# Optimization experiments

Measured on AMD Instinct MI355X. Metric: run time of the kernel, lower is better.

## Reference

```python
import jax, jax.numpy as jnp
import numpy as np

C_CURV = 0.01
K = 20
BALL_EPS = 4e-3  # hyptorch float32 boundary eps


def _e2p(x, c=C_CURV):
    # ToPoincare: expmap0 then project onto the Poincare ball
    sqrt_c = c ** 0.5
    n = jnp.maximum(jnp.linalg.norm(x, axis=-1, keepdims=True), 1e-15)
    y = jnp.tanh(sqrt_c * n) * x / (sqrt_c * n)
    maxnorm = (1.0 - BALL_EPS) / sqrt_c
    ny = jnp.maximum(jnp.linalg.norm(y, axis=-1, keepdims=True), 1e-15)
    return jnp.where(ny > maxnorm, y * (maxnorm / ny), y)


def _mobius_add(x, y, c=C_CURV):
    x2 = jnp.sum(x * x, axis=-1, keepdims=True)
    y2 = jnp.sum(y * y, axis=-1, keepdims=True)
    xy = jnp.sum(x * y, axis=-1, keepdims=True)
    num = (1.0 + 2.0 * c * xy + c * y2) * x + (1.0 - c * x2) * y
    den = 1.0 + 2.0 * c * xy + c * c * x2 * y2
    return num / jnp.maximum(den, 1e-15)


def _knn(x, k):
    # x: (B, C, N); Euclidean negative squared distance, topk indices
    inner = -2.0 * jnp.einsum('bcn,bcm->bnm', x, x)
    xx = jnp.sum(x * x, axis=1)  # (B, N)
    pd = -xx[:, :, None] - inner - xx[:, None, :]
    return jax.lax.top_k(pd, k)[1]  # (B, N, k)


def _graph_feature(x, k=K):
    # x: (B, C, N) -> (B, 2C, N, k)
    idx = _knn(x, k)
    xp = _e2p(jnp.transpose(x, (0, 2, 1)))  # (B, N, C) on Poincare ball
    feat = jax.vmap(lambda xb, ib: xb[ib])(xp, idx)  # (B, N, k, C) gather
    xc = jnp.broadcast_to(xp[:, :, None, :], feat.shape)
    out = jnp.concatenate([_mobius_add(feat, -xc), xc], axis=-1)
    return jnp.transpose(out, (0, 3, 1, 2))


def _bn(x, g, b, axes, eps=1e-5):
    # BatchNorm (training-mode batch statistics), channel axis = 1
    m = jnp.mean(x, axis=axes, keepdims=True)
    v = jnp.mean((x - m) ** 2, axis=axes, keepdims=True)
    shp = [1] * x.ndim
    shp[1] = -1
    return (x - m) / jnp.sqrt(v + eps) * g.reshape(shp) + b.reshape(shp)


def _ln(x, g, b, eps=1e-5):
    m = jnp.mean(x, axis=-1, keepdims=True)
    v = jnp.mean((x - m) ** 2, axis=-1, keepdims=True)
    return (x - m) / jnp.sqrt(v + eps) * g + b


def setup_inputs() -> dict:
    key = jax.random.key(0)
    ks = jax.random.split(key, 8)
    B, N, OUT = 16, 1024, 40
    s = 0.05
    return {
        'x': jax.random.normal(ks[0], (B, N, 3), jnp.float32),
        'conv1_w': jax.random.normal(ks[1], (64, 6), jnp.float32) * s,
        'bn1_g': jnp.ones((64,), jnp.float32), 'bn1_b': jnp.zeros((64,), jnp.float32),
        'conv2_w': jax.random.normal(ks[2], (192, 128), jnp.float32) * s,
        'bn2_g': jnp.ones((192,), jnp.float32), 'bn2_b': jnp.zeros((192,), jnp.float32),
        'conv3_w': jax.random.normal(ks[3], (1024, 256), jnp.float32) * s,
        'bn3_g': jnp.ones((1024,), jnp.float32), 'bn3_b': jnp.zeros((1024,), jnp.float32),
        'fc1_w': jax.random.normal(ks[4], (512, 1024), jnp.float32) * s,
        'fc1_b': jnp.zeros((512,), jnp.float32),
        'ln1_g': jnp.ones((512,), jnp.float32), 'ln1_b': jnp.zeros((512,), jnp.float32),
        'fc2_w': jax.random.normal(ks[5], (256, 512), jnp.float32) * s,
        'fc2_b': jnp.zeros((256,), jnp.float32),
        'ln2_g': jnp.ones((256,), jnp.float32), 'ln2_b': jnp.zeros((256,), jnp.float32),
        'out_w': jax.random.normal(ks[6], (OUT, 256), jnp.float32) * s,
        'out_b': jnp.zeros((OUT,), jnp.float32),
    }


def reference(x, conv1_w, bn1_g, bn1_b, conv2_w, bn2_g, bn2_b,
              conv3_w, bn3_g, bn3_b, fc1_w, fc1_b, ln1_g, ln1_b,
              fc2_w, fc2_b, ln2_g, ln2_b, out_w, out_b):
    xt = jnp.transpose(x, (0, 2, 1))  # (B, 3, N)
    f = _graph_feature(xt)            # (B, 6, N, k)
    h = jnp.einsum('oc,bcnk->bonk', conv1_w, f)
    h = jax.nn.relu(_bn(h, bn1_g, bn1_b, (0, 2, 3)))
    x1 = jnp.max(h, axis=-1)          # (B, 64, N)
    f = _graph_feature(x1)            # (B, 128, N, k)
    h = jnp.einsum('oc,bcnk->bonk', conv2_w, f)
    h = jax.nn.relu(_bn(h, bn2_g, bn2_b, (0, 2, 3)))
    x2 = jnp.max(h, axis=-1)          # (B, 192, N)
    h = jnp.concatenate([x1, x2], axis=1)  # (B, 256, N)
    h = jnp.einsum('oc,bcn->bon', conv3_w, h)
    h = jax.nn.relu(_bn(h, bn3_g, bn3_b, (0, 2)))
    h = jnp.max(h, axis=-1)           # (B, 1024)
    h = jax.nn.relu(_ln(h @ fc1_w.T + fc1_b, ln1_g, ln1_b))
    h = jax.nn.relu(_ln(h @ fc2_w.T + fc2_b, ln2_g, ln2_b))
    logits = h @ out_w.T + out_b      # (B, outdim)
    return jax.nn.log_softmax(logits, axis=1)
```

## Files before the change

kernel.cpp:

```cpp
#include <hip/hip_runtime.h>
#include <math.h>

#define B_ 16
#define N_ 1024
#define KNN 20
#define NPAIR (B_*N_)

typedef __attribute__((ext_vector_type(8))) short bf16x8;
typedef __attribute__((ext_vector_type(4))) float f32x4;

__device__ __forceinline__ unsigned fkey(float f) {
  unsigned u = __float_as_uint(f);
  return (u & 0x80000000u) ? ~u : (u | 0x80000000u);
}
__device__ __forceinline__ float fkeyinv(unsigned u) {
  unsigned b = (u & 0x80000000u) ? (u ^ 0x80000000u) : ~u;
  return __uint_as_float(b);
}
__device__ __forceinline__ unsigned short f2bf(float x) {
  unsigned u = __float_as_uint(x);
  unsigned r = (u + 0x7FFFu + ((u >> 16) & 1u)) >> 16;
  return (unsigned short)r;
}
__device__ __forceinline__ float bf2f(unsigned short u) {
  return __uint_as_float(((unsigned)u) << 16);
}
__device__ __forceinline__ unsigned knnkey(float d, int idx) {
  return (fkey(d) & 0xFFFFFC00u) | (unsigned)(1023 - idx);
}

__device__ __forceinline__ void topk_insert_u32(unsigned (&kl)[KNN], unsigned nk) {
  kl[KNN-1] = nk;
  #pragma unroll
  for (int i = KNN-1; i > 0; i--) {
    unsigned hi = max(kl[i-1], kl[i]);
    unsigned lo = min(kl[i-1], kl[i]);
    kl[i-1] = hi; kl[i] = lo;
  }
}

__device__ __forceinline__ int cnt_gt(const unsigned* __restrict__ L, unsigned v) {
  int j = 0;
  #pragma unroll
  for (int s = 16; s; s >>= 1) {
    int nj = j + s;
    if (nj <= KNN && L[nj-1] > v) j = nj;
  }
  return j;
}

__global__ void __launch_bounds__(256) k_prep_knn1(const float* __restrict__ x,
        float* __restrict__ xp1, const float* __restrict__ w2, const float* __restrict__ w3,
        unsigned short* __restrict__ w2h, unsigned short* __restrict__ wt3h,
        unsigned* __restrict__ keypart) {
  __shared__ float P[N_*3];
  __shared__ float XX[N_];
  if (blockIdx.x >= 512) {
    int i = (blockIdx.x - 512) * 256 + threadIdx.x;
    if (i < NPAIR) {
      float a0 = x[i*3+0], a1 = x[i*3+1], a2 = x[i*3+2];
      float n = sqrtf(a0*a0 + a1*a1 + a2*a2);
      n = fmaxf(n, 1e-15f);
      float th = tanhf(0.1f * n);
      float sc = th / (0.1f * n);
      float ny = fmaxf(th * 10.0f, 1e-15f);
      float mxn = (1.0f - 4e-3f) / 0.1f;
      if (ny > mxn) sc *= mxn / ny;
      xp1[i*3+0] = sc*a0; xp1[i*3+1] = sc*a1; xp1[i*3+2] = sc*a2;
    }
    if (i < 192*128) w2h[i] = f2bf(w2[i]);
    wt3h[i] = f2bf(w3[i]);
    return;
  }
  int blk = blockIdx.x;
  int b = blk >> 5, rc = (blk >> 3) & 3, cc = blk & 7;
  const float* xb = x + b*N_*3;
  for (int e = threadIdx.x; e < N_*3; e += 256) P[e] = xb[e];
  __syncthreads();
  for (int j = threadIdx.x; j < N_; j += 256) {
    float q0 = P[j*3], q1 = P[j*3+1], q2 = P[j*3+2];
    XX[j] = q0*q0 + q1*q1 + q2*q2;
  }
  __syncthreads();
  int r = rc*256 + threadIdx.x;
  float q0 = P[r*3], q1 = P[r*3+1], q2 = P[r*3+2];
  float xxq = XX[r];
  unsigned kl[KNN];
  #pragma unroll
  for (int i = 0; i < KNN; i++) kl[i] = 0u;
  int cbase = cc*128;
  for (int jj = 0; jj < 128; jj++) {
    int j = cbase + jj;
    float dot = q0*P[j*3] + q1*P[j*3+1] + q2*P[j*3+2];
    float d = 2.0f*dot - xxq - XX[j];
    unsigned nk = knnkey(d, j);
    if (nk > kl[KNN-1]) topk_insert_u32(kl, nk);
  }
  int p = b*N_ + r;
  unsigned* pe = keypart + (size_t)p*160 + cc*20;
  #pragma unroll
  for (int i = 0; i < KNN; i++) pe[i] = kl[i];
}

__global__ void __launch_bounds__(256) k_conv1(const float* __restrict__ xp1,
                        const unsigned* __restrict__ keypart,
                        const float* __restrict__ w1, float* __restrict__ hmax1,
                        float* __restrict__ hmin1, double* __restrict__ stats1sh) {
  __shared__ float F[4][KNN][6];
  __shared__ float red[4][64][2];
  __shared__ int idxs[16][KNN];
  __shared__ unsigned keybuf[2560];
  __shared__ unsigned out1[1280];
  __shared__ unsigned out2[640];
  int g = threadIdx.x >> 6, lane = threadIdx.x & 63;
  int tid = threadIdx.x;
  int pbase = blockIdx.x * 16;
  {
    const unsigned* src = keypart + (size_t)pbase*160;
    for (int e = tid; e < 2560; e += 256) keybuf[e] = src[e];
  }
  float w[6];
  #pragma unroll
  for (int c = 0; c < 6; c++) w[c] = w1[lane*6 + c];
  __syncthreads();
  for (int e = tid; e < 2560; e += 256) {
    int pt = e / 160, rem = e - pt*160;
    int m = rem / 40, i = rem - m*40;
    const unsigned* A = keybuf + pt*160 + (2*m)*20;
    const unsigned* Bl = A + 20;
    unsigned v; const unsigned* S; int own;
    if (i < 20) { v = A[i]; S = Bl; own = i; }
    else { v = Bl[i-20]; S = A; own = i-20; }
    int rank = own + cnt_gt(S, v);
    if (rank < KNN) out1[(pt*4 + m)*20 + rank] = v;
  }
  __syncthreads();
  for (int e = tid; e < 1280; e += 256) {
    int pt = e / 80, rem = e - pt*80;
    int m2 = rem / 40, i = rem - m2*40;
    const unsigned* A = out1 + (pt*4 + 2*m2)*20;
    const unsigned* Bl = A + 20;
    unsigned v; const unsigned* S; int own;
    if (i < 20) { v = A[i]; S = Bl; own = i; }
    else { v = Bl[i-20]; S = A; own = i-20; }
    int rank = own + cnt_gt(S, v);
    if (rank < KNN) out2[(pt*2 + m2)*20 + rank] = v;
  }
  __syncthreads();
  for (int e = tid; e < 640; e += 256) {
    int pt = e / 40, i = e - pt*40;
    const unsigned* A = out2 + pt*40;
    const unsigned* Bl = A + 20;
    unsigned v; const unsigned* S; int own;
    if (i < 20) { v = A[i]; S = Bl; own = i; }
    else { v = Bl[i-20]; S = A; own = i-20; }
    int rank = own + cnt_gt(S, v);
    if (rank < KNN) idxs[pt][rank] = 1023 - (int)(v & 1023u);
  }
  float sum = 0.f, sumsq = 0.f;
  __syncthreads();
  for (int it = 0; it < 4; ++it) {
    int p = pbase + it*4 + g;
    if (lane < KNN) {
      int nb = idxs[it*4 + g][lane];
      int bb = p >> 10;
      const float* xc = xp1 + p*3;
      const float* ft = xp1 + (bb*N_ + nb)*3;
      float x0 = ft[0], x1 = ft[1], x2v = ft[2];
      float c0 = xc[0], c1 = xc[1], c2 = xc[2];
      float X2 = x0*x0 + x1*x1 + x2v*x2v;
      float Y2 = c0*c0 + c1*c1 + c2*c2;
      float XY = -(x0*c0 + x1*c1 + x2v*c2);
      float den = fmaxf(1.0f + 0.02f*XY + 1e-4f*X2*Y2, 1e-15f);
      float s1 = (1.0f + 0.02f*XY + 0.01f*Y2) / den;
      float s2 = (1.0f - 0.01f*X2) / den;
      F[g][lane][0] = s1*x0 - s2*c0;
      F[g][lane][1] = s1*x1 - s2*c1;
      F[g][lane][2] = s1*x2v - s2*c2;
      F[g][lane][3] = c0; F[g][lane][4] = c1; F[g][lane][5] = c2;
    }
    __syncthreads();
    float mx = -__builtin_inff(), mn = __builtin_inff();
    for (int k = 0; k < KNN; k++) {
      float h = 0.f;
      #pragma unroll
      for (int c = 0; c < 6; c++) h = fmaf(w[c], F[g][k][c], h);
      mx = fmaxf(mx, h); mn = fminf(mn, h);
      sum += h; sumsq += h*h;
    }
    hmax1[(pbase + it*4 + g)*64 + lane] = mx;
    hmin1[(pbase + it*4 + g)*64 + lane] = mn;
    __syncthreads();
  }
  red[g][lane][0] = sum; red[g][lane][1] = sumsq;
  __syncthreads();
  if (g == 0) {
    float s  = red[0][lane][0] + red[1][lane][0] + red[2][lane][0] + red[3][lane][0];
    float s2 = red[0][lane][1] + red[1][lane][1] + red[2][lane][1] + red[3][lane][1];
    double* dst = stats1sh + ((size_t)(blockIdx.x & 63)*64 + lane)*2;
    atomicAdd(dst, (double)s);
    atomicAdd(dst + 1, (double)s2);
  }
}

__global__ void __launch_bounds__(64) k_bn_reduce(const double* __restrict__ sh, int nch, int nslots,
                            double cnt,
                            const float* __restrict__ g, const float* __restrict__ bb,
                            float* __restrict__ scale, float* __restrict__ shift) {
  int o = blockIdx.x, t = threadIdx.x;
  double s = 0.0, s2 = 0.0;
  for (int sl = t; sl < nslots; sl += 64) {
    s  += sh[((size_t)sl*nch + o)*2];
    s2 += sh[((size_t)sl*nch + o)*2 + 1];
  }
  #pragma unroll
  for (int off = 32; off > 0; off >>= 1) { s += __shfl_xor(s, off); s2 += __shfl_xor(s2, off); }
  if (t == 0) {
    double m = s / cnt;
    double v = s2 / cnt - m*m;
    float a = g[o] / sqrtf((float)v + 1e-5f);
    scale[o] = a;
    shift[o] = bb[o] - a * (float)m;
  }
}

__global__ void __launch_bounds__(256) k_bn1_apply(const float* __restrict__ hmax1, const float* __restrict__ hmin1,
                            const float* __restrict__ scale1, const float* __restrict__ shift1,
                            float* __restrict__ xp2,
                            unsigned short* __restrict__ x1h, unsigned short* __restrict__ x1l,
                            float* __restrict__ xx1) {
  int b = blockIdx.x >> 4, nc = blockIdx.x & 15;
  int c = threadIdx.x & 63, sub = threadIdx.x >> 6;
  int n0 = nc*64 + sub*16;
  float a = scale1[c], t = shift1[c];
  #pragma unroll
  for (int i = 0; i < 16; i++) {
    int p = b*1024 + n0 + i;
    float h = (a >= 0.f) ? hmax1[(size_t)p*64 + c] : hmin1[(size_t)p*64 + c];
    float x1 = fmaxf(fmaf(a, h, t), 0.f);
    unsigned short hb = f2bf(x1);
    x1h[(size_t)p*64 + c] = hb;
    x1l[(size_t)p*64 + c] = f2bf(x1 - bf2f(hb));
    float n2 = x1*x1;
    #pragma unroll
    for (int off = 32; off > 0; off >>= 1) n2 += __shfl_xor(n2, off);
    if (c == 0) xx1[p] = n2;
    float n1 = fmaxf(sqrtf(n2), 1e-15f);
    float th = tanhf(0.1f * n1);
    float sc = th / (0.1f * n1);
    float ny = fmaxf(th * 10.0f, 1e-15f);
    float mxn = (1.0f - 4e-3f) / 0.1f;
    if (ny > mxn) sc *= mxn / ny;
    xp2[(size_t)p*64 + c] = sc * x1;
  }
}

__global__ void __launch_bounds__(256) k_knn2g(const unsigned short* __restrict__ x1h,
        const unsigned short* __restrict__ x1l,
        const float* __restrict__ xx1, unsigned* __restrict__ keypart2) {
  __shared__ __align__(16) float SM[4096];
  int tid = threadIdx.x;
  int bi = blockIdx.x;
  int blk = ((bi & 7) << 7) + (bi >> 3);
  int b = blk >> 6, qc = (blk >> 2) & 15, cc = blk & 3;
  int qbase = qc*64, ccbase = cc*256;
  int wave = tid >> 6, lane = tid & 63;
  int lm = lane & 15, kq = lane >> 4;
  const size_t base = (size_t)b * 65536;

  bf16x8 Qh[4][2], Ql[4][2];
  #pragma unroll
  for (int qt = 0; qt < 4; qt++) {
    size_t ro = base + (size_t)(qbase + qt*16 + lm)*64 + kq*8;
    #pragma unroll
    for (int ks = 0; ks < 2; ks++) {
      Qh[qt][ks] = *((const bf16x8*)(x1h + ro + ks*32));
      Ql[qt][ks] = *((const bf16x8*)(x1l + ro + ks*32));
    }
  }
  unsigned kl[KNN];
  #pragma unroll
  for (int i = 0; i < KNN; i++) kl[i] = 0u;
  int cq = lane + (lane >> 2);

  for (int st = 0; st < 4; ++st) {
    int cb0 = ccbase + st*64;
    size_t co = base + (size_t)(cb0 + wave*16 + lm)*64 + kq*8;
    bf16x8 Ah[2], Al[2];
    #pragma unroll
    for (int ks = 0; ks < 2; ks++) {
      Ah[ks] = *((const bf16x8*)(x1h + co + ks*32));
      Al[ks] = *((const bf16x8*)(x1l + co + ks*32));
    }
    float4 xxc = *((const float4*)(xx1 + b*1024 + cb0 + wave*16 + kq*4));
    f32x4 acc[4];
    #pragma unroll
    for (int qt = 0; qt < 4; qt++) acc[qt] = (f32x4){0.f, 0.f, 0.f, 0.f};
    #pragma unroll
    for (int ks = 0; ks < 2; ks++) {
      #pragma unroll
      for (int qt = 0; qt < 4; qt++) {
        acc[qt] = __builtin_amdgcn_mfma_f32_16x16x32_bf16(Ah[ks], Qh[qt][ks], acc[qt], 0, 0, 0);
        acc[qt] = __builtin_amdgcn_mfma_f32_16x16x32_bf16(Ah[ks], Ql[qt][ks], acc[qt], 0, 0, 0);
        acc[qt] = __builtin_amdgcn_mfma_f32_16x16x32_bf16(Al[ks], Qh[qt][ks], acc[qt], 0, 0, 0);
        acc[qt] = __builtin_amdgcn_mfma_f32_16x16x32_bf16(Al[ks], Ql[qt][ks], acc[qt], 0, 0, 0);
      }
    }
    __syncthreads();
    float xxcv[4] = {xxc.x, xxc.y, xxc.z, xxc.w};
    #pragma unroll
    for (int qt = 0; qt < 4; qt++) {
      int q = qt*16 + lm;
      #pragma unroll
      for (int r = 0; r < 4; r++) {
        int c = wave*16 + kq*4 + r;
        SM[q*64 + ((c + q + (q>>2)) & 63)] = 2.0f*acc[qt][r] - xxcv[r];
      }
    }
    __syncthreads();
    #pragma unroll
    for (int j = 0; j < 16; j++) {
      int c = wave*16 + j;
      float d = SM[lane*64 + ((c + cq) & 63)];
      unsigned nk = knnkey(d, cb0 + c);
      if (nk > kl[KNN-1]) topk_insert_u32(kl, nk);
    }
  }
  __syncthreads();
  unsigned* U = (unsigned*)SM;
  unsigned* L0 = U;
  unsigned* L1 = U + 1344;
  unsigned* M  = U + 2688;
  if (wave == 0) {
    #pragma unroll
    for (int i = 0; i < KNN; i++) L0[lane*21 + i] = kl[i];
  } else if (wave == 1) {
    #pragma unroll
    for (int i = 0; i < KNN; i++) L1[lane*21 + i] = kl[i];
  }
  __syncthreads();
  if (tid < 64) {
    int ia = 0, ib = 0;
    for (int t = 0; t < KNN; t++) {
      unsigned pa = L0[tid*21 + ia], pb = L1[tid*21 + ib];
      bool ta = pa > pb;
      M[tid*21 + t] = ta ? pa : pb;
      if (ta) ia++; else ib++;
    }
  }
  __syncthreads();
  if (wave == 2) {
    #pragma unroll
    for (int i = 0; i < KNN; i++) L0[lane*21 + i] = kl[i];
  } else if (wave == 3) {
    #pragma unroll
    for (int i = 0; i < KNN; i++) L1[lane*21 + i] = kl[i];
  }
  __syncthreads();
  if (tid < 64) {
    int p = b*N_ + qbase + tid;
    unsigned* pe = keypart2 + (size_t)p*80 + cc*20;
    int ia = 0, ib = 0, im = 0;
    for (int t = 0; t < KNN; t++) {
      unsigned pa = L0[tid*21 + ia], pb = L1[tid*21 + ib], pm = M[tid*21 + im];
      unsigned bp = pm; int sel = 2;
      if (pa > bp) { bp = pa; sel = 0; }
      if (pb > bp) { bp = pb; sel = 1; }
      pe[t] = bp;
      if (sel == 0) ia++; else if (sel == 1) ib++; else im++;
    }
  }
}

__global__ void __launch_bounds__(256) k_conv2m(const float* __restrict__ xp2,
    const unsigned* __restrict__ keypart2, const unsigned short* __restrict__ w2h,
    float* __restrict__ hmax2, float* __restrict__ hmin2, double* __restrict__ stats2sh) {
  __shared__ __align__(16) short Abf[80*136];
  __shared__ __align__(16) float Cf[4][64];
  __shared__ float Yc[4];
  __shared__ int nbr[80];
  __shared__ unsigned keybuf[320];
  int tid = threadIdx.x;
  int bi = blockIdx.x;
  int g512 = ((bi & 7) << 9) + (bi >> 3);
  int p0 = g512 * 4;
  int b = p0 >> 10;
  for (int e = tid; e < 320; e += 256) keybuf[e] = keypart2[(size_t)p0*80 + e];
  if (tid < 64) {
    int pt = tid >> 4, qq = tid & 15;
    float4 cv = *((const float4*)(xp2 + (size_t)(p0 + pt)*64) + qq);
    *((float4*)&Cf[pt][qq*4]) = cv;
    float y2 = cv.x*cv.x + cv.y*cv.y + cv.z*cv.z + cv.w*cv.w;
    #pragma unroll
    for (int off = 8; off > 0; off >>= 1) y2 += __shfl_xor(y2, off);
    if (qq == 0) Yc[pt] = y2;
    ushort4 cb;
    cb.x = f2bf(cv.x); cb.y = f2bf(cv.y); cb.z = f2bf(cv.z); cb.w = f2bf(cv.w);
    #pragma unroll
    for (int a = 0; a < 5; a++)
      #pragma unroll
      for (int j2 = 0; j2 < 4; j2++)
        *((ushort4*)(Abf + (a*16 + pt*4 + j2)*136 + 64 + qq*4)) = cb;
  }
  __syncthreads();
  for (int e = tid; e < 320; e += 256) {
    int pt = e / 80;
    int rem = e - pt*80;
    int c = rem / 20;
    int i = rem - c*20;
    const unsigned* LB = keybuf + pt*80;
    unsigned v = LB[c*20 + i];
    int rank = i;
    #pragma unroll
    for (int c2 = 0; c2 < 4; c2++) {
      if (c2 == c) continue;
      rank += cnt_gt(LB + c2*20, v);
    }
    if (rank < KNN) nbr[pt*20 + rank] = 1023 - (int)(v & 1023u);
  }
  __syncthreads();
  for (int e = tid; e < 80*16; e += 256) {
    int r = e >> 4, qq = e & 15;
    int q = (r >> 2) & 3;
    int L = 20*q + 4*(r >> 4) + (r & 3);
    float4 f = *((const float4*)(xp2 + (size_t)(b*N_ + nbr[L])*64) + qq);
    float4 cvf = *((const float4*)&Cf[q][qq*4]);
    float X2 = f.x*f.x + f.y*f.y + f.z*f.z + f.w*f.w;
    float XY = -(f.x*cvf.x + f.y*cvf.y + f.z*cvf.z + f.w*cvf.w);
    #pragma unroll
    for (int off = 8; off > 0; off >>= 1) {
      X2 += __shfl_xor(X2, off);
      XY += __shfl_xor(XY, off);
    }
    float Y2 = Yc[q];
    float den = fmaxf(1.0f + 0.02f*XY + 1e-4f*X2*Y2, 1e-15f);
    float inv = 1.0f / den;
    float s1 = (1.0f + 0.02f*XY + 0.01f*Y2) * inv;
    float s2 = (1.0f - 0.01f*X2) * inv;
    ushort4 mo;
    mo.x = f2bf(s1*f.x - s2*cvf.x);
    mo.y = f2bf(s1*f.y - s2*cvf.y);
    mo.z = f2bf(s1*f.z - s2*cvf.z);
    mo.w = f2bf(s1*f.w - s2*cvf.w);
    *((ushort4*)(Abf + r*136 + qq*4)) = mo;
  }
  __syncthreads();
  int wave = tid >> 6, lane = tid & 63;
  int quad = lane >> 4, lm = lane & 15;
  int colbase = wave*48;
  f32x4 acc[5][3];
  #pragma unroll
  for (int rt = 0; rt < 5; rt++)
    #pragma unroll
    for (int cj = 0; cj < 3; cj++) acc[rt][cj] = (f32x4){0.f, 0.f, 0.f, 0.f};
  #pragma unroll
  for (int kt = 0; kt < 4; kt++) {
    int k0 = kt*32 + quad*8;
    bf16x8 bf[3];
    #pragma unroll
    for (int cj = 0; cj < 3; cj++)
      bf[cj] = *((const bf16x8*)(w2h + (size_t)(colbase + cj*16 + lm)*128 + k0));
    bf16x8 af[5];
    #pragma unroll
    for (int rt = 0; rt < 5; rt++)
      af[rt] = *((const bf16x8*)(Abf + (rt*16 + lm)*136 + k0));
    #pragma unroll
    for (int rt = 0; rt < 5; rt++)
      #pragma unroll
      for (int cj = 0; cj < 3; cj++)
        acc[rt][cj] = __builtin_amdgcn_mfma_f32_16x16x32_bf16(af[rt], bf[cj], acc[rt][cj], 0, 0, 0);
  }
  #pragma unroll
  for (int cj = 0; cj < 3; cj++) {
    int o = colbase + cj*16 + lm;
    float s = 0.f, s2 = 0.f, mx = -__builtin_inff(), mn = __builtin_inff();
    #pragma unroll
    for (int rt = 0; rt < 5; rt++) {
      #pragma unroll
      for (int reg = 0; reg < 4; reg++) {
        float h = acc[rt][cj][reg];
        s += h; s2 += h*h;
        mx = fmaxf(mx, h); mn = fminf(mn, h);
      }
    }
    hmax2[(size_t)(p0 + quad)*192 + o] = mx;
    hmin2[(size_t)(p0 + quad)*192 + o] = mn;
    s  += __shfl_xor(s, 16);  s  += __shfl_xor(s, 32);
    s2 += __shfl_xor(s2, 16); s2 += __shfl_xor(s2, 32);
    if (lane < 16) {
      double* dst = stats2sh + ((size_t)(bi & 255)*192 + o)*2;
      atomicAdd(dst, (double)s); atomicAdd(dst + 1, (double)s2);
    }
  }
}

__global__ void __launch_bounds__(256) k_conv3m(
   const float* __restrict__ hmax1, const float* __restrict__ hmin1,
   const float* __restrict__ scale1, const float* __restrict__ shift1,
   const float* __restrict__ hmax2, const float* __restrict__ hmin2,
   const float* __restrict__ scale2, const float* __restrict__ shift2,
   const unsigned short* __restrict__ wt3h, double* __restrict__ stats3sh,
   unsigned* __restrict__ hmax3u, unsigned* __restrict__ hmin3u) {
  __shared__ short As[64*264];
  int tid = threadIdx.x;
  int mt = blockIdx.x >> 2, cb = blockIdx.x & 3;
  int rowbase = mt*64;
  int b = rowbase >> 10;
  int c4 = tid & 63;
  float4 sc, sh;
  if (c4 < 16) {
    sc = *((const float4*)(scale1 + c4*4));
    sh = *((const float4*)(shift1 + c4*4));
  } else {
    sc = *((const float4*)(scale2 + (c4*4 - 64)));
    sh = *((const float4*)(shift2 + (c4*4 - 64)));
  }
  #pragma unroll 4
  for (int i = 0; i < 16; i++) {
    int r = (tid >> 6) + i*4;
    int p = rowbase + r;
    float4 hx, hn;
    if (c4 < 16) {
      hx = *((const float4*)(hmax1 + (size_t)p*64 + c4*4));
      hn = *((const float4*)(hmin1 + (size_t)p*64 + c4*4));
    } else {
      hx = *((const float4*)(hmax2 + (size_t)p*192 + (c4*4 - 64)));
      hn = *((const float4*)(hmin2 + (size_t)p*192 + (c4*4 - 64)));
    }
    ushort4 o4;
    o4.x = f2bf(fmaxf(fmaf(sc.x, (sc.x >= 0.f ? hx.x : hn.x), sh.x), 0.f));
    o4.y = f2bf(fmaxf(fmaf(sc.y, (sc.y >= 0.f ? hx.y : hn.y), sh.y), 0.f));
    o4.z = f2bf(fmaxf(fmaf(sc.z, (sc.z >= 0.f ? hx.z : hn.z), sh.z), 0.f));
    o4.w = f2bf(fmaxf(fmaf(sc.w, (sc.w >= 0.f ? hx.w : hn.w), sh.w), 0.f));
    *((ushort4*)(As + r*264 + c4*4)) = o4;
  }
  __syncthreads();
  int wave = tid >> 6, lane = tid & 63;
  int quad = lane >> 4, lm = lane & 15;
  int colbase = cb*256 + wave*64;
  f32x4 acc[4][4];
  #pragma unroll
  for (int ri = 0; ri < 4; ri++)
    #pragma unroll
    for (int cj = 0; cj < 4; cj++) acc[ri][cj] = (f32x4){0.f, 0.f, 0.f, 0.f};
  for (int kt = 0; kt < 8; kt++) {
    int k0 = kt*32 + quad*8;
    bf16x8 bf[4];
    #pragma unroll
    for (int cj = 0; cj < 4; cj++)
      bf[cj] = *((const bf16x8*)(wt3h + (size_t)(colbase + cj*16 + lm)*256 + k0));
    bf16x8 af[4];
    #pragma unroll
    for (int ri = 0; ri < 4; ri++)
      af[ri] = *((const bf16x8*)(As + (ri*16 + lm)*264 + k0));
    #pragma unroll
    for (int ri = 0; ri < 4; ri++)
      #pragma unroll
      for (int cj = 0; cj < 4; cj++)
        acc[ri][cj] = __builtin_amdgcn_mfma_f32_16x16x32_bf16(af[ri], bf[cj], acc[ri][cj], 0, 0, 0);
  }
  #pragma unroll
  for (int cj = 0; cj < 4; cj++) {
    float s = 0.f, s2 = 0.f, mx = -__builtin_inff(), mn = __builtin_inff();
    #pragma unroll
    for (int ri = 0; ri < 4; ri++) {
      #pragma unroll
      for (int reg = 0; reg < 4; reg++) {
        float h = acc[ri][cj][reg];
        s += h; s2 += h*h; mx = fmaxf(mx, h); mn = fminf(mn, h);
      }
    }
    s  += __shfl_xor(s, 16);  s  += __shfl_xor(s, 32);
    s2 += __shfl_xor(s2, 16); s2 += __shfl_xor(s2, 32);
    mx = fmaxf(mx, __shfl_xor(mx, 16)); mx = fmaxf(mx, __shfl_xor(mx, 32));
    mn = fminf(mn, __shfl_xor(mn, 16)); mn = fminf(mn, __shfl_xor(mn, 32));
    if (lane < 16) {
      int col = colbase + cj*16 + lane;
      double* dst = stats3sh + ((size_t)(blockIdx.x & 63)*1024 + col)*2;
      atomicAdd(dst, (double)s);
      atomicAdd(dst + 1, (double)s2);
      atomicMax(hmax3u + b*1024 + col, fkey(mx));
      atomicMin(hmin3u + b*1024 + col, fkey(mn));
    }
  }
}

__device__ float blk_reduce(float v, float* red, int tid) {
  red[tid] = v; __syncthreads();
  for (int st = 128; st > 0; st >>= 1) {
    if (tid < st) red[tid] += red[tid + st];
    __syncthreads();
  }
  float r = red[0]; __syncthreads();
  return r;
}

__global__ void __launch_bounds__(256) k_head1(const unsigned* __restrict__ hmax3u,
    const unsigned* __restrict__ hmin3u,
    const float* __restrict__ scale3, const float* __restrict__ shift3,
    const float* __restrict__ fc1w, const float* __restrict__ fc1b,
    float* __restrict__ h1buf) {
  __shared__ __align__(16) float V[1024];
  int b = blockIdx.x >> 5, oc = blockIdx.x & 31;
  int tid = threadIdx.x;
  for (int o = tid; o < 1024; o += 256) {
    float a = scale3[o];
    unsigned u = (a >= 0.f) ? hmax3u[b*1024 + o] : hmin3u[b*1024 + o];
    V[o] = fmaxf(fmaf(a, fkeyinv(u), shift3[o]), 0.f);
  }
  __syncthreads();
  int ty = tid >> 4, tx = tid & 15;
  int o = oc*16 + ty;
  const float4* wr = (const float4*)(fc1w + (size_t)o*1024) + tx*16;
  const float4* vv = (const float4*)V + tx*16;
  float s = 0.f;
  #pragma unroll
  for (int i = 0; i < 16; i++) {
    float4 w = wr[i]; float4 v = vv[i];
    s = fmaf(w.x, v.x, s); s = fmaf(w.y, v.y, s);
    s = fmaf(w.z, v.z, s); s = fmaf(w.w, v.w, s);
  }
  s += __shfl_xor(s, 1); s += __shfl_xor(s, 2);
  s += __shfl_xor(s, 4); s += __shfl_xor(s, 8);
  if (tx == 0) h1buf[b*512 + o] = s + fc1b[o];
}

__global__ void __launch_bounds__(256) k_head2(const float* __restrict__ h1buf,
    const float* __restrict__ ln1g, const float* __restrict__ ln1b,
    const float* __restrict__ fc2w, const float* __restrict__ fc2b,
    float* __restrict__ h2buf) {
  __shared__ __align__(16) float H1[512];
  __shared__ float red[256];
  int b = blockIdx.x >> 3, oc = blockIdx.x & 7;
  int tid = threadIdx.x;
  float v0 = h1buf[b*512 + tid], v1 = h1buf[b*512 + 256 + tid];
  float s = blk_reduce(v0 + v1, red, tid);
  float s2 = blk_reduce(v0*v0 + v1*v1, red, tid);
  float m = s / 512.f;
  float var = s2 / 512.f - m*m;
  float inv = 1.0f / sqrtf(var + 1e-5f);
  H1[tid] = fmaxf((v0 - m)*inv*ln1g[tid] + ln1b[tid], 0.f);
  H1[256 + tid] = fmaxf((v1 - m)*inv*ln1g[256 + tid] + ln1b[256 + tid], 0.f);
  __syncthreads();
  int ty = tid >> 3, tx = tid & 7;
  int o = oc*32 + ty;
  const float4* wr = (const float4*)(fc2w + (size_t)o*512) + tx*16;
  const float4* vv = (const float4*)H1 + tx*16;
  float t = 0.f;
  #pragma unroll
  for (int i = 0; i < 16; i++) {
    float4 w = wr[i]; float4 v = vv[i];
    t = fmaf(w.x, v.x, t); t = fmaf(w.y, v.y, t);
    t = fmaf(w.z, v.z, t); t = fmaf(w.w, v.w, t);
  }
  t += __shfl_xor(t, 1); t += __shfl_xor(t, 2); t += __shfl_xor(t, 4);
  if (tx == 0) h2buf[b*256 + o] = t + fc2b[o];
}

__global__ void __launch_bounds__(256) k_head3(const float* __restrict__ h2buf,
    const float* __restrict__ ln2g, const float* __restrict__ ln2b,
    const float* __restrict__ outw, const float* __restrict__ outb,
    float* __restrict__ out) {
  __shared__ __align__(16) float H2[256];
  __shared__ float red[256];
  int b = blockIdx.x, tid = threadIdx.x;
  float h2v = h2buf[b*256 + tid];
  float ss = blk_reduce(h2v, red, tid);
  float ss2 = blk_reduce(h2v*h2v, red, tid);
  float m2 = ss / 256.f;
  float var2 = ss2 / 256.f - m2*m2;
  float inv2 = 1.0f / sqrtf(var2 + 1e-5f);
  H2[tid] = fmaxf((h2v - m2)*inv2*ln2g[tid] + ln2b[tid], 0.f);
  __syncthreads();
  if (tid < 40) {
    const float4* wr = (const float4*)(outw + (size_t)tid*256);
    float t = 0.f;
    for (int c4 = 0; c4 < 64; c4++) {
      float4 w = wr[c4]; float4 vv = ((const float4*)H2)[c4];
      t = fmaf(w.x, vv.x, t); t = fmaf(w.y, vv.y, t);
      t = fmaf(w.z, vv.z, t); t = fmaf(w.w, vv.w, t);
    }
    red[tid] = t + outb[tid];
  }
  __syncthreads();
  if (tid == 0) {
    float mx = -__builtin_inff();
    for (int i2 = 0; i2 < 40; i2++) mx = fmaxf(mx, red[i2]);
    float se = 0.f;
    for (int i2 = 0; i2 < 40; i2++) se += expf(red[i2] - mx);
    float lse = mx + logf(se);
    for (int i2 = 0; i2 < 40; i2++) out[b*40 + i2] = red[i2] - lse;
  }
}

extern "C" void kernel_launch(void* const* d_in, const int* in_sizes, int n_in,
                              void* d_out, int out_size, void* d_ws, size_t ws_size,
                              hipStream_t stream) {
  (void)in_sizes; (void)n_in; (void)out_size; (void)ws_size;
  const float* x    = (const float*)d_in[0];
  const float* w1   = (const float*)d_in[1];
  const float* bn1g = (const float*)d_in[2];
  const float* bn1b = (const float*)d_in[3];
  const float* w2   = (const float*)d_in[4];
  const float* bn2g = (const float*)d_in[5];
  const float* bn2b = (const float*)d_in[6];
  const float* w3   = (const float*)d_in[7];
  const float* bn3g = (const float*)d_in[8];
  const float* bn3b = (const float*)d_in[9];
  const float* fc1w = (const float*)d_in[10];
  const float* fc1b = (const float*)d_in[11];
  const float* ln1g = (const float*)d_in[12];
  const float* ln1b = (const float*)d_in[13];
  const float* fc2w = (const float*)d_in[14];
  const float* fc2b = (const float*)d_in[15];
  const float* ln2g = (const float*)d_in[16];
  const float* ln2b = (const float*)d_in[17];
  const float* outw = (const float*)d_in[18];
  const float* outb = (const float*)d_in[19];
  float* out = (float*)d_out;

  float* ws = (float*)d_ws;
  size_t off = 0;
  float* xp1   = ws + off; off += 49152;
  float* hmax1 = ws + off; off += 1048576;
  float* hmin1 = ws + off; off += 1048576;
  float* xp2   = ws + off; off += 1048576;
  float* hmax2 = ws + off; off += 3145728;
  float* hmin2 = ws + off; off += 3145728;
  unsigned* keypart2 = (unsigned*)(ws + off); off += 1310720;
  unsigned short* w2h = (unsigned short*)(ws + off); off += 24576;
  unsigned short* wt3h = (unsigned short*)(ws + off); off += 131072;
  float* x1bf  = ws + off; off += 1048576;
  float* xx1   = ws + off; off += 16384;
  float* h1buf = ws + off; off += 8192;
  float* h2buf = ws + off; off += 4096;
  float* scale1 = ws + off; off += 64;
  float* shift1 = ws + off; off += 64;
  float* scale2 = ws + off; off += 192;
  float* shift2 = ws + off; off += 192;
  float* scale3 = ws + off; off += 1024;
  float* shift3 = ws + off; off += 1024;
  double* stats1sh = (double*)(ws + off);
  double* stats2sh = stats1sh + 64*64*2;
  double* stats3sh = stats2sh + (size_t)256*192*2;
  unsigned* hmax3u = (unsigned*)(stats3sh + (size_t)64*1024*2);
  unsigned* hmin3u = hmax3u + 16384;
  unsigned* keypartA = (unsigned*)hmax2;
  unsigned short* x1h = (unsigned short*)x1bf;
  unsigned short* x1l = x1h + 1048576;

  size_t zero_bytes = ((size_t)64*64*2 + (size_t)256*192*2 + (size_t)64*1024*2)*8 + (size_t)16384*4;
  hipMemsetAsync(stats1sh, 0, zero_bytes, stream);
  hipMemsetAsync(hmin3u, 0xFF, (size_t)16384*4, stream);

  k_prep_knn1<<<1536, 256, 0, stream>>>(x, xp1, w2, w3, w2h, wt3h, keypartA);
  k_conv1<<<1024, 256, 0, stream>>>(xp1, keypartA, w1, hmax1, hmin1, stats1sh);
  k_bn_reduce<<<64, 64, 0, stream>>>(stats1sh, 64, 64, 327680.0, bn1g, bn1b, scale1, shift1);
  k_bn1_apply<<<256, 256, 0, stream>>>(hmax1, hmin1, scale1, shift1, xp2, x1h, x1l, xx1);
  k_knn2g<<<1024, 256, 0, stream>>>(x1h, x1l, xx1, keypart2);
  k_conv2m<<<4096, 256, 0, stream>>>(xp2, keypart2, w2h, hmax2, hmin2, stats2sh);
  k_bn_reduce<<<192, 64, 0, stream>>>(stats2sh, 192, 256, 327680.0, bn2g, bn2b, scale2, shift2);
  k_conv3m<<<1024, 256, 0, stream>>>(hmax1, hmin1, scale1, shift1, hmax2, hmin2, scale2, shift2,
                                     wt3h, stats3sh, hmax3u, hmin3u);
  k_bn_reduce<<<1024, 64, 0, stream>>>(stats3sh, 1024, 64, 16384.0, bn3g, bn3b, scale3, shift3);
  k_head1<<<512, 256, 0, stream>>>(hmax3u, hmin3u, scale3, shift3, fc1w, fc1b, h1buf);
  k_head2<<<128, 256, 0, stream>>>(h1buf, ln1g, ln1b, fc2w, fc2b, h2buf);
  k_head3<<<16, 256, 0, stream>>>(h2buf, ln2g, ln2b, outw, outb, out);
}
```

Before: 361.5 us.

## Store conv2 max/min in fp16, use float stat atomics, reuse bf16 x1

```diff
diff --git a/kernel.cpp b/kernel.cpp
--- a/kernel.cpp
+++ b/kernel.cpp
@@ -24,6 +24,14 @@
 }
 __device__ __forceinline__ float bf2f(unsigned short u) {
   return __uint_as_float(((unsigned)u) << 16);
+}
+__device__ __forceinline__ unsigned short f2h(float x) {
+  _Float16 h = (_Float16)x;
+  return *(unsigned short*)&h;
+}
+__device__ __forceinline__ float h2f(unsigned short u) {
+  _Float16 h = *(_Float16*)&u;
+  return (float)h;
 }
 __device__ __forceinline__ unsigned knnkey(float d, int idx) {
   return (fkey(d) & 0xFFFFFC00u) | (unsigned)(1023 - idx);
@@ -105,7 +113,7 @@
 __global__ void __launch_bounds__(256) k_conv1(const float* __restrict__ xp1,
                         const unsigned* __restrict__ keypart,
                         const float* __restrict__ w1, float* __restrict__ hmax1,
-                        float* __restrict__ hmin1, double* __restrict__ stats1sh) {
+                        float* __restrict__ hmin1, float* __restrict__ stats1sh) {
   __shared__ float F[4][KNN][6];
   __shared__ float red[4][64][2];
   __shared__ int idxs[16][KNN];
@@ -197,21 +205,21 @@
   if (g == 0) {
     float s  = red[0][lane][0] + red[1][lane][0] + red[2][lane][0] + red[3][lane][0];
     float s2 = red[0][lane][1] + red[1][lane][1] + red[2][lane][1] + red[3][lane][1];
-    double* dst = stats1sh + ((size_t)(blockIdx.x & 63)*64 + lane)*2;
-    atomicAdd(dst, (double)s);
-    atomicAdd(dst + 1, (double)s2);
-  }
-}
-
-__global__ void __launch_bounds__(64) k_bn_reduce(const double* __restrict__ sh, int nch, int nslots,
+    float* dst = stats1sh + ((size_t)(blockIdx.x & 63)*64 + lane)*2;
+    atomicAdd(dst, s);
+    atomicAdd(dst + 1, s2);
+  }
+}
+
+__global__ void __launch_bounds__(64) k_bn_reduce(const float* __restrict__ sh, int nch, int nslots,
                             double cnt,
                             const float* __restrict__ g, const float* __restrict__ bb,
                             float* __restrict__ scale, float* __restrict__ shift) {
   int o = blockIdx.x, t = threadIdx.x;
   double s = 0.0, s2 = 0.0;
   for (int sl = t; sl < nslots; sl += 64) {
-    s  += sh[((size_t)sl*nch + o)*2];
-    s2 += sh[((size_t)sl*nch + o)*2 + 1];
+    s  += (double)sh[((size_t)sl*nch + o)*2];
+    s2 += (double)sh[((size_t)sl*nch + o)*2 + 1];
   }
   #pragma unroll
   for (int off = 32; off > 0; off >>= 1) { s += __shfl_xor(s, off); s2 += __shfl_xor(s2, off); }
@@ -374,7 +382,8 @@
 
 __global__ void __launch_bounds__(256) k_conv2m(const float* __restrict__ xp2,
     const unsigned* __restrict__ keypart2, const unsigned short* __restrict__ w2h,
-    float* __restrict__ hmax2, float* __restrict__ hmin2, double* __restrict__ stats2sh) {
+    unsigned short* __restrict__ hmax2, unsigned short* __restrict__ hmin2,
+    float* __restrict__ stats2sh) {
   __shared__ __align__(16) short Abf[80*136];
   __shared__ __align__(16) float Cf[4][64];
   __shared__ float Yc[4];
@@ -483,23 +492,22 @@
         mx = fmaxf(mx, h); mn = fminf(mn, h);
       }
     }
-    hmax2[(size_t)(p0 + quad)*192 + o] = mx;
-    hmin2[(size_t)(p0 + quad)*192 + o] = mn;
+    hmax2[(size_t)(p0 + quad)*192 + o] = f2h(mx);
+    hmin2[(size_t)(p0 + quad)*192 + o] = f2h(mn);
     s  += __shfl_xor(s, 16);  s  += __shfl_xor(s, 32);
     s2 += __shfl_xor(s2, 16); s2 += __shfl_xor(s2, 32);
     if (lane < 16) {
-      double* dst = stats2sh + ((size_t)(bi & 255)*192 + o)*2;
-      atomicAdd(dst, (double)s); atomicAdd(dst + 1, (double)s2);
+      float* dst = stats2sh + ((size_t)(bi & 255)*192 + o)*2;
+      atomicAdd(dst, s); atomicAdd(dst + 1, s2);
     }
   }
 }
 
 __global__ void __launch_bounds__(256) k_conv3m(
-   const float* __restrict__ hmax1, const float* __restrict__ hmin1,
-   const float* __restrict__ scale1, const float* __restrict__ shift1,
-   const float* __restrict__ hmax2, const float* __restrict__ hmin2,
+   const unsigned short* __restrict__ x1h,
+   const unsigned short* __restrict__ hmax2, const unsigned short* __restrict__ hmin2,
    const float* __restrict__ scale2, const float* __restrict__ shift2,
-   const unsigned short* __restrict__ wt3h, double* __restrict__ stats3sh,
+   const unsigned short* __restrict__ wt3h, float* __restrict__ stats3sh,
    unsigned* __restrict__ hmax3u, unsigned* __restrict__ hmin3u) {
   __shared__ short As[64*264];
   int tid = threadIdx.x;
@@ -508,10 +516,7 @@
   int b = rowbase >> 10;
   int c4 = tid & 63;
   float4 sc, sh;
-  if (c4 < 16) {
-    sc = *((const float4*)(scale1 + c4*4));
-    sh = *((const float4*)(shift1 + c4*4));
-  } else {
+  if (c4 >= 16) {
     sc = *((const float4*)(scale2 + (c4*4 - 64)));
     sh = *((const float4*)(shift2 + (c4*4 - 64)));
   }
@@ -519,20 +524,19 @@
   for (int i = 0; i < 16; i++) {
     int r = (tid >> 6) + i*4;
     int p = rowbase + r;
-    float4 hx, hn;
     if (c4 < 16) {
-      hx = *((const float4*)(hmax1 + (size_t)p*64 + c4*4));
-      hn = *((const float4*)(hmin1 + (size_t)p*64 + c4*4));
+      *((ushort4*)(As + r*264 + c4*4)) =
+        *((const ushort4*)(x1h + (size_t)p*64 + c4*4));
     } else {
-      hx = *((const float4*)(hmax2 + (size_t)p*192 + (c4*4 - 64)));
-      hn = *((const float4*)(hmin2 + (size_t)p*192 + (c4*4 - 64)));
-    }
-    ushort4 o4;
-    o4.x = f2bf(fmaxf(fmaf(sc.x, (sc.x >= 0.f ? hx.x : hn.x), sh.x), 0.f));
-    o4.y = f2bf(fmaxf(fmaf(sc.y, (sc.y >= 0.f ? hx.y : hn.y), sh.y), 0.f));
-    o4.z = f2bf(fmaxf(fmaf(sc.z, (sc.z >= 0.f ? hx.z : hn.z), sh.z), 0.f));
-    o4.w = f2bf(fmaxf(fmaf(sc.w, (sc.w >= 0.f ? hx.w : hn.w), sh.w), 0.f));
-    *((ushort4*)(As + r*264 + c4*4)) = o4;
+      ushort4 hx4 = *((const ushort4*)(hmax2 + (size_t)p*192 + (c4*4 - 64)));
+      ushort4 hn4 = *((const ushort4*)(hmin2 + (size_t)p*192 + (c4*4 - 64)));
+      ushort4 o4;
+      o4.x = f2bf(fmaxf(fmaf(sc.x, (sc.x >= 0.f ? h2f(hx4.x) : h2f(hn4.x)), sh.x), 0.f));
+      o4.y = f2bf(fmaxf(fmaf(sc.y, (sc.y >= 0.f ? h2f(hx4.y) : h2f(hn4.y)), sh.y), 0.f));
+      o4.z = f2bf(fmaxf(fmaf(sc.z, (sc.z >= 0.f ? h2f(hx4.z) : h2f(hn4.z)), sh.z), 0.f));
+      o4.w = f2bf(fmaxf(fmaf(sc.w, (sc.w >= 0.f ? h2f(hx4.w) : h2f(hn4.w)), sh.w), 0.f));
+      *((ushort4*)(As + r*264 + c4*4)) = o4;
+    }
   }
   __syncthreads();
   int wave = tid >> 6, lane = tid & 63;
@@ -576,9 +580,9 @@
     mn = fminf(mn, __shfl_xor(mn, 16)); mn = fminf(mn, __shfl_xor(mn, 32));
     if (lane < 16) {
       int col = colbase + cj*16 + lane;
-      double* dst = stats3sh + ((size_t)(blockIdx.x & 63)*1024 + col)*2;
-      atomicAdd(dst, (double)s);
-      atomicAdd(dst + 1, (double)s2);
+      float* dst = stats3sh + ((size_t)(blockIdx.x & 63)*1024 + col)*2;
+      atomicAdd(dst, s);
+      atomicAdd(dst + 1, s2);
       atomicMax(hmax3u + b*1024 + col, fkey(mx));
       atomicMin(hmin3u + b*1024 + col, fkey(mn));
     }
@@ -725,8 +729,8 @@
   float* hmax1 = ws + off; off += 1048576;
   float* hmin1 = ws + off; off += 1048576;
   float* xp2   = ws + off; off += 1048576;
-  float* hmax2 = ws + off; off += 3145728;
-  float* hmin2 = ws + off; off += 3145728;
+  float* hmax2f = ws + off; off += 3145728;
+  float* hmin2f = ws + off; off += 3145728;
   unsigned* keypart2 = (unsigned*)(ws + off); off += 1310720;
   unsigned short* w2h = (unsigned short*)(ws + off); off += 24576;
   unsigned short* wt3h = (unsigned short*)(ws + off); off += 131072;
@@ -740,16 +744,18 @@
   float* shift2 = ws + off; off += 192;
   float* scale3 = ws + off; off += 1024;
   float* shift3 = ws + off; off += 1024;
-  double* stats1sh = (double*)(ws + off);
-  double* stats2sh = stats1sh + 64*64*2;
-  double* stats3sh = stats2sh + (size_t)256*192*2;
+  float* stats1sh = ws + off;
+  float* stats2sh = stats1sh + 64*64*2;
+  float* stats3sh = stats2sh + (size_t)256*192*2;
   unsigned* hmax3u = (unsigned*)(stats3sh + (size_t)64*1024*2);
   unsigned* hmin3u = hmax3u + 16384;
-  unsigned* keypartA = (unsigned*)hmax2;
+  unsigned* keypartA = (unsigned*)hmax2f;
   unsigned short* x1h = (unsigned short*)x1bf;
   unsigned short* x1l = x1h + 1048576;
-
-  size_t zero_bytes = ((size_t)64*64*2 + (size_t)256*192*2 + (size_t)64*1024*2)*8 + (size_t)16384*4;
+  unsigned short* hmax2 = (unsigned short*)hmax2f;
+  unsigned short* hmin2 = (unsigned short*)hmin2f;
+
+  size_t zero_bytes = ((size_t)64*64*2 + (size_t)256*192*2 + (size_t)64*1024*2)*4 + (size_t)16384*4;
   hipMemsetAsync(stats1sh, 0, zero_bytes, stream);
   hipMemsetAsync(hmin3u, 0xFF, (size_t)16384*4, stream);
 
@@ -760,7 +766,7 @@
   k_knn2g<<<1024, 256, 0, stream>>>(x1h, x1l, xx1, keypart2);
   k_conv2m<<<4096, 256, 0, stream>>>(xp2, keypart2, w2h, hmax2, hmin2, stats2sh);
   k_bn_reduce<<<192, 64, 0, stream>>>(stats2sh, 192, 256, 327680.0, bn2g, bn2b, scale2, shift2);
-  k_conv3m<<<1024, 256, 0, stream>>>(hmax1, hmin1, scale1, shift1, hmax2, hmin2, scale2, shift2,
+  k_conv3m<<<1024, 256, 0, stream>>>(x1h, hmax2, hmin2, scale2, shift2,
                                      wt3h, stats3sh, hmax3u, hmin3u);
   k_bn_reduce<<<1024, 64, 0, stream>>>(stats3sh, 1024, 64, 16384.0, bn3g, bn3b, scale3, shift3);
   k_head1<<<512, 256, 0, stream>>>(hmax3u, hmin3u, scale3, shift3, fc1w, fc1b, h1buf);
```

Result: faster. 345.7 us (-4.3%).
